# Kernel optimization log

Measured on AMD Instinct MI355X. Metric: run time of the kernel, lower is better.

The kernel has to match this reference:

```python
import jax, jax.numpy as jnp
import numpy as np

D = 1024

def _layernorm(x, gamma, beta, eps=1e-5):
    mu = jnp.mean(x, axis=-1, keepdims=True)
    var = jnp.var(x, axis=-1, keepdims=True)
    return (x - mu) * jax.lax.rsqrt(var + eps) * gamma + beta

def setup_inputs() -> dict:
    key = jax.random.key(0)
    ks = jax.random.split(key, 8)
    B, S = 4, 4096
    hidden_states = jax.random.normal(ks[0], (B, S, D), dtype=jnp.float32)
    attention_mask = jnp.ones((B, S), dtype=jnp.int32)  # unused by the module
    scale = 0.02
    Wq = jax.random.normal(ks[1], (D, D), jnp.float32) * scale
    bq = jnp.zeros((D,), jnp.float32)
    Wk = jax.random.normal(ks[2], (D, D), jnp.float32) * scale
    bk = jnp.zeros((D,), jnp.float32)
    Wv = jax.random.normal(ks[3], (D, D), jnp.float32) * scale
    bv = jnp.zeros((D,), jnp.float32)
    # query_att / key_att are initialized to weight=0, bias=1 in the module
    Wqa = jnp.zeros((D, D), jnp.float32)
    bqa = jnp.ones((D,), jnp.float32)
    Wka = jnp.zeros((D, D), jnp.float32)
    bka = jnp.ones((D,), jnp.float32)
    gamma = jnp.ones((D,), jnp.float32)
    beta = jnp.zeros((D,), jnp.float32)
    return {"hidden_states": hidden_states, "attention_mask": attention_mask,
            "Wq": Wq, "bq": bq, "Wqa": Wqa, "bqa": bqa,
            "Wk": Wk, "bk": bk, "Wka": Wka, "bka": bka,
            "Wv": Wv, "bv": bv, "gamma": gamma, "beta": beta}

def reference(hidden_states, attention_mask, Wq, bq, Wqa, bqa, Wk, bk, Wka, bka, Wv, bv, gamma, beta):
    h = _layernorm(hidden_states, gamma, beta)  # (B,S,D)
    B, S, d_model = h.shape
    inv_sqrt_d = 1.0 / jnp.sqrt(jnp.float32(d_model))
    query = h @ Wq + bq
    keys = h @ Wk + bk
    values = h @ Wv + bv
    # cumulative mean scaling: 1..S
    scaling = jnp.arange(1, S + 1, dtype=h.dtype).reshape(1, S, 1)
    query_weight = jax.nn.softmax((query @ Wqa + bqa) * inv_sqrt_d, axis=-1)
    pooled_query = jnp.cumsum(query_weight * query, axis=1) / scaling
    mixed_keys = pooled_query * keys
    keys_weight = jax.nn.softmax((mixed_keys @ Wka + bka) * inv_sqrt_d, axis=-1)
    pooled_keys = jnp.cumsum(keys_weight * mixed_keys, axis=1) / scaling
    return pooled_keys * values
```

## Files before the change

kernel.cpp:

```cpp
#include <hip/hip_runtime.h>

typedef _Float16 half_t;
typedef _Float16 f16x8 __attribute__((ext_vector_type(8)));
typedef _Float16 f16x4 __attribute__((ext_vector_type(4)));
typedef float f32x4 __attribute__((ext_vector_type(4)));

#define D_MODEL 1024
#define BS 4
#define SEQ 4096
#define ROWS (BS * SEQ)
#define SC 128
#define NC (SEQ / SC)

#define BARRIER() asm volatile("s_barrier" ::: "memory")
#define WAITV(n)  asm volatile("s_waitcnt vmcnt(" #n ")" ::: "memory")

__device__ __forceinline__ void gld_lds16(const half_t* g, char* l) {
  __builtin_amdgcn_global_load_lds((const __attribute__((address_space(1))) void*)g,
                                   (__attribute__((address_space(3))) void*)l, 16, 0, 0);
}

__global__ void zero_flags(int* f) {
  if (threadIdx.x < 2) f[threadIdx.x] = 0;
}

__global__ __launch_bounds__(256) void detect_nz(const float* __restrict__ W0,
                                                 const float* __restrict__ W1,
                                                 int* __restrict__ flags) {
  const int which = blockIdx.x >> 8;
  const unsigned* w = (const unsigned*)(which ? W1 : W0);
  const int blk = blockIdx.x & 255;
  unsigned v = 0;
  const size_t base = (size_t)blk * 4096 + threadIdx.x;
#pragma unroll
  for (int i = 0; i < 16; ++i) v |= w[base + i * 256];
#pragma unroll
  for (int off = 32; off > 0; off >>= 1) v |= __shfl_down(v, off, 64);
  __shared__ unsigned sv[4];
  if ((threadIdx.x & 63) == 0) sv[threadIdx.x >> 6] = v;
  __syncthreads();
  if (threadIdx.x == 0) {
    v = sv[0] | sv[1] | sv[2] | sv[3];
    if (v) atomicOr(&flags[which], 1);
  }
}

__global__ __launch_bounds__(256) void bias_softmax(const float* __restrict__ bqa,
                                                    const float* __restrict__ bka,
                                                    float* __restrict__ qwv,
                                                    float* __restrict__ kwv) {
  const float* b = blockIdx.x ? bka : bqa;
  float* o = blockIdx.x ? kwv : qwv;
  const int t = threadIdx.x;
  f32x4 v = *(const f32x4*)(b + t * 4);
  float x[4];
#pragma unroll
  for (int i = 0; i < 4; i++) x[i] = v[i] * 0.03125f;
  float mx = fmaxf(fmaxf(x[0], x[1]), fmaxf(x[2], x[3]));
#pragma unroll
  for (int off = 32; off > 0; off >>= 1) mx = fmaxf(mx, __shfl_xor(mx, off, 64));
  __shared__ float sm[4], ssum[4];
  const int wv = t >> 6, ln = t & 63;
  if (ln == 0) sm[wv] = mx;
  __syncthreads();
  mx = fmaxf(fmaxf(sm[0], sm[1]), fmaxf(sm[2], sm[3]));
  float e[4]; float s = 0.f;
#pragma unroll
  for (int i = 0; i < 4; i++) { e[i] = expf(x[i] - mx); s += e[i]; }
#pragma unroll
  for (int off = 32; off > 0; off >>= 1) s += __shfl_xor(s, off, 64);
  if (ln == 0) ssum[wv] = s;
  __syncthreads();
  s = ssum[0] + ssum[1] + ssum[2] + ssum[3];
  const float r = 1.0f / s;
  f32x4 ov;
#pragma unroll
  for (int i = 0; i < 4; i++) ov[i] = e[i] * r;
  *(f32x4*)(o + t * 4) = ov;
}

__global__ __launch_bounds__(256) void ln_kernel(const float* __restrict__ x,
                                                 const float* __restrict__ gamma,
                                                 const float* __restrict__ beta,
                                                 half_t* __restrict__ h) {
  const int row = blockIdx.x;
  const int t = threadIdx.x;
  const float* xr = x + (size_t)row * D_MODEL + t * 4;
  f32x4 v = *(const f32x4*)xr;
  float s = v[0] + v[1] + v[2] + v[3];
  float q = v[0]*v[0] + v[1]*v[1] + v[2]*v[2] + v[3]*v[3];
#pragma unroll
  for (int off = 32; off > 0; off >>= 1) {
    s += __shfl_down(s, off, 64);
    q += __shfl_down(q, off, 64);
  }
  __shared__ float rs[4], rq[4];
  const int wv = t >> 6, ln = t & 63;
  if (ln == 0) { rs[wv] = s; rq[wv] = q; }
  __syncthreads();
  s = rs[0] + rs[1] + rs[2] + rs[3];
  q = rq[0] + rq[1] + rq[2] + rq[3];
  const float mu = s * (1.0f / D_MODEL);
  const float var = q * (1.0f / D_MODEL) - mu * mu;
  const float rstd = rsqrtf(var + 1e-5f);
  f32x4 g = *(const f32x4*)(gamma + t * 4);
  f32x4 b = *(const f32x4*)(beta + t * 4);
  f16x4 o;
#pragma unroll
  for (int i = 0; i < 4; i++) o[i] = (half_t)((v[i] - mu) * rstd * g[i] + b[i]);
  *(f16x4*)(h + (size_t)row * D_MODEL + t * 4) = o;
}

__global__ __launch_bounds__(256) void prep_w(const float* __restrict__ Wq,
                                              const float* __restrict__ Wk,
                                              const float* __restrict__ Wv,
                                              const float* __restrict__ Wqa,
                                              const float* __restrict__ Wka,
                                              half_t* __restrict__ wcat,
                                              half_t* __restrict__ wqa,
                                              half_t* __restrict__ wka) {
  const int b = blockIdx.x;
  const int mat = b >> 10;
  const int tile = b & 1023;
  const int tn = (tile & 31) * 32;
  const int tk = (tile >> 5) * 32;
  const float* W = mat == 0 ? Wq : mat == 1 ? Wk : mat == 2 ? Wv : mat == 3 ? Wqa : Wka;
  half_t* dst = mat < 3 ? wcat + (size_t)mat * D_MODEL * D_MODEL : (mat == 3 ? wqa : wka);
  __shared__ float tl[32][33];
  const int tx = threadIdx.x & 31, ty = threadIdx.x >> 5;
#pragma unroll
  for (int i = 0; i < 32; i += 8)
    tl[ty + i][tx] = W[(size_t)(tk + ty + i) * D_MODEL + tn + tx];
  __syncthreads();
#pragma unroll
  for (int i = 0; i < 32; i += 8)
    dst[(size_t)(tn + ty + i) * D_MODEL + tk + tx] = (half_t)tl[tx][ty + i];
}

__global__ __launch_bounds__(256) void copy_bias(const float* __restrict__ bq,
                                                 const float* __restrict__ bk,
                                                 const float* __restrict__ bv,
                                                 float* __restrict__ bcat) {
  const int i = blockIdx.x * 256 + threadIdx.x;
  if (i < 1024) bcat[i] = bq[i];
  else if (i < 2048) bcat[i] = bk[i - 1024];
  else if (i < 3072) bcat[i] = bv[i - 2048];
}


#define STAGE_A(buf, h, kt) do { \
  gld_lds16(gA + (size_t)(h)*128*lda + (size_t)(kt)*64,        smem + (buf)*65536 + (h)*16384 + wid*1024); \
  gld_lds16(gA + ((size_t)(h)*128 + 64)*lda + (size_t)(kt)*64, smem + (buf)*65536 + (h)*16384 + 8192 + wid*1024); \
} while (0)

#define STAGE_B(buf, h, kt) do { \
  gld_lds16(gB + (size_t)(h)*128*1024 + (size_t)(kt)*64,        smem + (buf)*65536 + 32768 + (h)*16384 + wid*1024); \
  gld_lds16(gB + ((size_t)(h)*128 + 64)*1024 + (size_t)(kt)*64, smem + (buf)*65536 + 32768 + (h)*16384 + 8192 + wid*1024); \
} while (0)

#define LOAD_A(buf, base) do { \
  _Pragma("unroll") for (int _fm = 0; _fm < 4; ++_fm) { \
    aF[_fm][0] = *(const f16x8*)(smem + (buf)*65536 + rA + gsw0 + ((base)+_fm)*2048); \
    aF[_fm][1] = *(const f16x8*)(smem + (buf)*65536 + rA + gsw1 + ((base)+_fm)*2048); \
  } \
} while (0)

#define LOAD_B(dst, buf, base) do { \
  _Pragma("unroll") for (int _fn = 0; _fn < 2; ++_fn) { \
    dst[_fn][0] = *(const f16x8*)(smem + (buf)*65536 + 32768 + rB + gsw0 + ((base)+_fn)*2048); \
    dst[_fn][1] = *(const f16x8*)(smem + (buf)*65536 + 32768 + rB + gsw1 + ((base)+_fn)*2048); \
  } \
} while (0)

#define QUAD(BR, MOFF, NOFF) do { \
  __builtin_amdgcn_s_setprio(1); \
  _Pragma("unroll") for (int _fm = 0; _fm < 4; ++_fm) \
  _Pragma("unroll") for (int _fn = 0; _fn < 2; ++_fn) { \
    acc[(MOFF)+_fm][(NOFF)+_fn] = __builtin_amdgcn_mfma_f32_16x16x32_f16(aF[_fm][0], BR[_fn][0], acc[(MOFF)+_fm][(NOFF)+_fn], 0, 0, 0); \
    acc[(MOFF)+_fm][(NOFF)+_fn] = __builtin_amdgcn_mfma_f32_16x16x32_f16(aF[_fm][1], BR[_fn][1], acc[(MOFF)+_fm][(NOFF)+_fn], 0, 0, 0); \
  } \
  __builtin_amdgcn_s_setprio(0); \
} while (0)

__global__ __launch_bounds__(512, 2) void gemm8(const half_t* __restrict__ A, int lda,
                                                const half_t* __restrict__ Bt,
                                                const float* __restrict__ bias,
                                                half_t* __restrict__ C, int ldc,
                                                const int* skip) {
  if (skip && *skip == 0) return;
  extern __shared__ char smem[];
  const int t = threadIdx.x;
  const int ln = t & 63, wid = t >> 6;
  const int wm = wid >> 2, wn = wid & 3;

  const int gx = gridDim.x;
  const int nwg = gx * gridDim.y;
  const int orig = blockIdx.y * gx + blockIdx.x;
  const int swz = (orig & 7) * (nwg >> 3) + (orig >> 3);
  const int bx = swz % gx, by = swz / gx;
  const int n0 = bx * 256, m0 = by * 256;

  const int srow = t >> 3;
  const int sg = (t & 7) ^ (srow & 7);
  const half_t* gA = A + (size_t)(m0 + srow) * lda + sg * 8;
  const half_t* gB = Bt + (size_t)(n0 + srow) * 1024 + sg * 8;

  const int rA = (wm * 128 + (ln & 15)) * 128;
  const int rB = (wn * 64 + (ln & 15)) * 128;
  const int gsw0 = (((ln >> 4)) ^ (ln & 7)) << 4;
  const int gsw1 = ((4 | (ln >> 4)) ^ (ln & 7)) << 4;

  f32x4 acc[8][4] = {};
  f16x8 aF[4][2], bL[2][2], bH[2][2];

  STAGE_B(0, 0, 0); STAGE_B(0, 1, 0); STAGE_A(0, 0, 0); STAGE_A(0, 1, 0);
  STAGE_B(1, 0, 1); STAGE_B(1, 1, 1); STAGE_A(1, 0, 1); STAGE_A(1, 1, 1);
  WAITV(8); BARRIER();

#pragma unroll 1
  for (int i = 0; i < 8; ++i) {
    const int kc = 2 * i + 2;
    const int kd = 2 * i + 3;
    const bool f = (i < 7);
    LOAD_A(0, 0);
    LOAD_B(bL, 0, 0);
    BARRIER(); QUAD(bL, 0, 0); BARRIER();
    LOAD_B(bH, 0, 2);
    BARRIER(); QUAD(bH, 0, 2); BARRIER();
    LOAD_A(0, 4);
    if (f) { STAGE_B(0, 0, kc); STAGE_B(0, 1, kc); }
    BARRIER(); QUAD(bH, 4, 2); BARRIER();
    if (f) { STAGE_A(0, 0, kc); STAGE_A(0, 1, kc); WAITV(8); } else WAITV(0);
    BARRIER(); QUAD(bL, 4, 0); BARRIER();
    LOAD_A(1, 0);
    LOAD_B(bL, 1, 0);
    BARRIER(); QUAD(bL, 0, 0); BARRIER();
    LOAD_B(bH, 1, 2);
    BARRIER(); QUAD(bH, 0, 2); BARRIER();
    LOAD_A(1, 4);
    if (f) { STAGE_B(1, 0, kd); STAGE_B(1, 1, kd); }
    BARRIER(); QUAD(bH, 4, 2); BARRIER();
    if (f) { STAGE_A(1, 0, kd); STAGE_A(1, 1, kd); WAITV(8); } else WAITV(0);
    BARRIER(); QUAD(bL, 4, 0); BARRIER();
  }

  const int r0 = m0 + wm * 128 + ((ln >> 4) << 2);
  const int c0 = n0 + wn * 64 + (ln & 15);
  float bb[4];
#pragma unroll
  for (int fn = 0; fn < 4; ++fn) bb[fn] = bias[c0 + fn * 16];
#pragma unroll
  for (int fm = 0; fm < 8; ++fm)
#pragma unroll
    for (int fn = 0; fn < 4; ++fn) {
      const int col = c0 + fn * 16;
      const int row = r0 + fm * 16;
#pragma unroll
      for (int r = 0; r < 4; ++r)
        C[(size_t)(row + r) * ldc + col] = (half_t)(acc[fm][fn][r] + bb[fn]);
    }
}

__global__ __launch_bounds__(256) void softmax_k(const half_t* __restrict__ L,
                                                 half_t* __restrict__ O,
                                                 const int* skip) {
  if (skip && *skip == 0) return;
  const size_t row = blockIdx.x;
  const int t = threadIdx.x;
  f16x4 v = *(const f16x4*)(L + row * D_MODEL + t * 4);
  float x[4];
#pragma unroll
  for (int i = 0; i < 4; i++) x[i] = (float)v[i] * 0.03125f;
  float mx = fmaxf(fmaxf(x[0], x[1]), fmaxf(x[2], x[3]));
#pragma unroll
  for (int off = 32; off > 0; off >>= 1) mx = fmaxf(mx, __shfl_xor(mx, off, 64));
  __shared__ float sm[4], ssum[4];
  const int wv = t >> 6, ln = t & 63;
  if (ln == 0) sm[wv] = mx;
  __syncthreads();
  mx = fmaxf(fmaxf(sm[0], sm[1]), fmaxf(sm[2], sm[3]));
  float e[4]; float s = 0.f;
#pragma unroll
  for (int i = 0; i < 4; i++) { e[i] = expf(x[i] - mx); s += e[i]; }
#pragma unroll
  for (int off = 32; off > 0; off >>= 1) s += __shfl_xor(s, off, 64);
  if (ln == 0) ssum[wv] = s;
  __syncthreads();
  s = ssum[0] + ssum[1] + ssum[2] + ssum[3];
  const float r = 1.0f / s;
  f16x4 o;
#pragma unroll
  for (int i = 0; i < 4; i++) o[i] = (half_t)(e[i] * r);
  *(f16x4*)(O + row * D_MODEL + t * 4) = o;
}

__global__ __launch_bounds__(256) void cs_partial(const int* __restrict__ nz,
                                                  const float* __restrict__ wv,
                                                  const half_t* __restrict__ A, int ldA,
                                                  const half_t* __restrict__ B, int ldB,
                                                  float* __restrict__ part) {
  const int d = blockIdx.x * 256 + threadIdx.x;
  const int c = blockIdx.y;
  const int bb = blockIdx.z;
  const size_t s0 = (size_t)bb * SEQ + (size_t)c * SC;
  const half_t* pa = A + s0 * ldA + d;
  const half_t* pb = B + s0 * ldB + d;
  float acc = 0.f;
  if (*nz == 0) {
    const float w = wv[d];
#pragma unroll 8
    for (int s = 0; s < SC; s++) acc += w * (float)pb[(size_t)s * ldB];
  } else {
#pragma unroll 8
    for (int s = 0; s < SC; s++) acc += (float)pa[(size_t)s * ldA] * (float)pb[(size_t)s * ldB];
  }
  part[((size_t)bb * NC + c) * D_MODEL + d] = acc;
}

__global__ __launch_bounds__(256) void cs_partial2(const int* __restrict__ nz,
                                                   const float* __restrict__ wv,
                                                   const float* __restrict__ msum,
                                                   const half_t* __restrict__ A, int ldA,
                                                   const half_t* __restrict__ B, int ldB,
                                                   float* __restrict__ part) {
  const int d = blockIdx.x * 256 + threadIdx.x;
  const int c = blockIdx.y;
  const int bb = blockIdx.z;
  const size_t idx = ((size_t)bb * NC + c) * D_MODEL + d;
  if (*nz == 0) {
    part[idx] = wv[d] * msum[idx];
    return;
  }
  const size_t s0 = (size_t)bb * SEQ + (size_t)c * SC;
  const half_t* pa = A + s0 * ldA + d;
  const half_t* pb = B + s0 * ldB + d;
  float acc = 0.f;
#pragma unroll 8
  for (int s = 0; s < SC; s++) acc += (float)pa[(size_t)s * ldA] * (float)pb[(size_t)s * ldB];
  part[idx] = acc;
}

template <bool HALF_OUT>
__global__ __launch_bounds__(256) void cs_apply(const int* __restrict__ nz,
                                                const float* __restrict__ wv,
                                                const half_t* __restrict__ A, int ldA,
                                                const half_t* __restrict__ B, int ldB,
                                                const half_t* __restrict__ Cm, int ldC,
                                                const float* __restrict__ part,
                                                float* __restrict__ msum,
                                                half_t* __restrict__ OH,
                                                float* __restrict__ OF) {
  const int d = blockIdx.x * 256 + threadIdx.x;
  const int c = blockIdx.y;
  const int bb = blockIdx.z;
  float acc = 0.f;
  for (int cc = 0; cc < c; cc++) acc += part[((size_t)bb * NC + cc) * D_MODEL + d];
  const size_t s0 = (size_t)bb * SEQ + (size_t)c * SC;
  float ms = 0.f;
  if (*nz == 0) {
    const float w = wv[d];
#pragma unroll 4
    for (int s = 0; s < SC; s++) {
      const size_t sg = s0 + s;
      acc += w * (float)B[sg * ldB + d];
      const float pooled = acc / (float)(c * SC + s + 1);
      const float m = pooled * (float)Cm[sg * ldC + d];
      ms += m;
      if (HALF_OUT) OH[sg * D_MODEL + d] = (half_t)m;
      else          OF[sg * D_MODEL + d] = m;
    }
  } else {
#pragma unroll 4
    for (int s = 0; s < SC; s++) {
      const size_t sg = s0 + s;
      acc += (float)A[sg * ldA + d] * (float)B[sg * ldB + d];
      const float pooled = acc / (float)(c * SC + s + 1);
      const float m = pooled * (float)Cm[sg * ldC + d];
      ms += m;
      if (HALF_OUT) OH[sg * D_MODEL + d] = (half_t)m;
      else          OF[sg * D_MODEL + d] = m;
    }
  }
  if (msum) msum[((size_t)bb * NC + c) * D_MODEL + d] = ms;
}

extern "C" void kernel_launch(void* const* d_in, const int* in_sizes, int n_in,
                              void* d_out, int out_size, void* d_ws, size_t ws_size,
                              hipStream_t stream) {
  const float* x     = (const float*)d_in[0];
  const float* Wq    = (const float*)d_in[2];
  const float* bq    = (const float*)d_in[3];
  const float* Wqa   = (const float*)d_in[4];
  const float* bqa   = (const float*)d_in[5];
  const float* Wk    = (const float*)d_in[6];
  const float* bk    = (const float*)d_in[7];
  const float* Wka   = (const float*)d_in[8];
  const float* bka   = (const float*)d_in[9];
  const float* Wv    = (const float*)d_in[10];
  const float* bv    = (const float*)d_in[11];
  const float* gamma = (const float*)d_in[12];
  const float* beta  = (const float*)d_in[13];
  float* out = (float*)d_out;

  char* ws = (char*)d_ws;
  const size_t MB = 1024 * 1024;
  half_t* h16    = (half_t*)(ws + 0);
  half_t* qkv16  = (half_t*)(ws + 32 * MB);
  half_t* logits = (half_t*)(ws + 128 * MB);
  half_t* wcat   = (half_t*)(ws + 160 * MB);
  half_t* wqa16  = (half_t*)(ws + 166 * MB);
  half_t* wka16  = (half_t*)(ws + 168 * MB);
  float*  bcat   = (float*)(ws + 170 * MB);
  float*  part   = (float*)(ws + 170 * MB + 64 * 1024);
  float*  msum   = (float*)(ws + 170 * MB + 1024 * 1024);
  float*  qwv    = (float*)(ws + 170 * MB + 1600 * 1024);
  float*  kwv    = (float*)(ws + 170 * MB + 1604 * 1024);
  int*    flags  = (int*)(ws + 170 * MB + 1608 * 1024);

  half_t* q16 = qkv16;
  half_t* k16 = qkv16 + 1024;
  half_t* v16 = qkv16 + 2048;
  half_t* mixed16 = h16;
  half_t* sw = logits;

  hipFuncSetAttribute((const void*)gemm8, hipFuncAttributeMaxDynamicSharedMemorySize, 131072);

  zero_flags<<<1, 64, 0, stream>>>(flags);
  detect_nz<<<512, 256, 0, stream>>>(Wqa, Wka, flags);
  bias_softmax<<<2, 256, 0, stream>>>(bqa, bka, qwv, kwv);
  prep_w<<<5120, 256, 0, stream>>>(Wq, Wk, Wv, Wqa, Wka, wcat, wqa16, wka16);
  copy_bias<<<12, 256, 0, stream>>>(bq, bk, bv, bcat);
  ln_kernel<<<ROWS, 256, 0, stream>>>(x, gamma, beta, h16);
  gemm8<<<dim3(12, 64), 512, 131072, stream>>>(h16, 1024, wcat, bcat, qkv16, 3072, nullptr);
  gemm8<<<dim3(4, 64), 512, 131072, stream>>>(q16, 3072, wqa16, bqa, logits, 1024, flags);
  softmax_k<<<ROWS, 256, 0, stream>>>(logits, sw, flags);
  cs_partial<<<dim3(4, NC, BS), 256, 0, stream>>>(flags, qwv, sw, 1024, q16, 3072, part);
  cs_apply<true><<<dim3(4, NC, BS), 256, 0, stream>>>(flags, qwv, sw, 1024, q16, 3072,
                                                      k16, 3072, part, msum, mixed16, nullptr);
  gemm8<<<dim3(4, 64), 512, 131072, stream>>>(mixed16, 1024, wka16, bka, logits, 1024, flags + 1);
  softmax_k<<<ROWS, 256, 0, stream>>>(logits, sw, flags + 1);
  cs_partial2<<<dim3(4, NC, BS), 256, 0, stream>>>(flags + 1, kwv, msum, sw, 1024,
                                                   mixed16, 1024, part);
  cs_apply<false><<<dim3(4, NC, BS), 256, 0, stream>>>(flags + 1, kwv, sw, 1024, mixed16, 1024,
                                                       v16, 3072, part, nullptr, nullptr, out);
}
```

Baseline: 225.3 us.

## Interleave finer-grained global-to-LDS staging across GEMM compute phases

The GEMM's global-to-LDS prefetch is reorganised. Each wave now stages a contiguous 8-row group with a per-row XOR swizzle, and the A and B tile halves are issued in smaller pieces spread across all eight compute quads. Part of the next buffer's B tile is deferred into the following iteration, and the vmcnt waits are tightened to match. The aim is to overlap memory traffic more evenly with MFMA work and avoid bursts of outstanding loads. The cost is a more fragile dependency schedule between staging, waits and LDS reads.

```diff
diff --git a/kernel.cpp b/kernel.cpp
--- a/kernel.cpp
+++ b/kernel.cpp
@@ -148,14 +148,18 @@
 }
 
 
-#define STAGE_A(buf, h, kt) do { \
-  gld_lds16(gA + (size_t)(h)*128*lda + (size_t)(kt)*64,        smem + (buf)*65536 + (h)*16384 + wid*1024); \
-  gld_lds16(gA + ((size_t)(h)*128 + 64)*lda + (size_t)(kt)*64, smem + (buf)*65536 + (h)*16384 + 8192 + wid*1024); \
+#define SA2(buf, rb, kt) do { \
+  gld_lds16(gA + (size_t)((rb) + wbA + r8) * lda + (size_t)(kt) * 64 + grn * 8, \
+            smem + (buf)*65536 + ((rb) + wbA) * 128); \
+  gld_lds16(gA + (size_t)((rb) + 128 + wbA + r8) * lda + (size_t)(kt) * 64 + grn * 8, \
+            smem + (buf)*65536 + ((rb) + 128 + wbA) * 128); \
 } while (0)
 
-#define STAGE_B(buf, h, kt) do { \
-  gld_lds16(gB + (size_t)(h)*128*1024 + (size_t)(kt)*64,        smem + (buf)*65536 + 32768 + (h)*16384 + wid*1024); \
-  gld_lds16(gB + ((size_t)(h)*128 + 64)*1024 + (size_t)(kt)*64, smem + (buf)*65536 + 32768 + (h)*16384 + 8192 + wid*1024); \
+#define SB2(buf, gd, kt) do { \
+  gld_lds16(gB + (size_t)((gd) + wbB + r8) * 1024 + (size_t)(kt) * 64 + grn * 8, \
+            smem + (buf)*65536 + 32768 + ((gd) + wbB) * 128); \
+  gld_lds16(gB + (size_t)((gd) + 128 + wbB + r8) * 1024 + (size_t)(kt) * 64 + grn * 8, \
+            smem + (buf)*65536 + 32768 + ((gd) + 128 + wbB) * 128); \
 } while (0)
 
 #define LOAD_A(buf, base) do { \
@@ -200,10 +204,12 @@
   const int bx = swz % gx, by = swz / gx;
   const int n0 = bx * 256, m0 = by * 256;
 
-  const int srow = t >> 3;
-  const int sg = (t & 7) ^ (srow & 7);
-  const half_t* gA = A + (size_t)(m0 + srow) * lda + sg * 8;
-  const half_t* gB = Bt + (size_t)(n0 + srow) * 1024 + sg * 8;
+  const int r8 = (t >> 3) & 7;
+  const int grn = (t & 7) ^ r8;
+  const int wbA = wid * 8;
+  const int wbB = ((wid >> 2) << 6) + (wid & 3) * 8;
+  const half_t* gA = A + (size_t)m0 * lda;
+  const half_t* gB = Bt + (size_t)n0 * 1024;
 
   const int rA = (wm * 128 + (ln & 15)) * 128;
   const int rB = (wn * 64 + (ln & 15)) * 128;
@@ -213,34 +219,37 @@
   f32x4 acc[8][4] = {};
   f16x8 aF[4][2], bL[2][2], bH[2][2];
 
-  STAGE_B(0, 0, 0); STAGE_B(0, 1, 0); STAGE_A(0, 0, 0); STAGE_A(0, 1, 0);
-  STAGE_B(1, 0, 1); STAGE_B(1, 1, 1); STAGE_A(1, 0, 1); STAGE_A(1, 1, 1);
-  WAITV(8); BARRIER();
+  SA2(0, 0, 0); SB2(0, 0, 0); SA2(0, 64, 0); SB2(0, 32, 0);
+  SA2(1, 0, 1); SB2(1, 0, 1); SA2(1, 64, 1);
+  WAITV(6); BARRIER();
 
 #pragma unroll 1
   for (int i = 0; i < 8; ++i) {
+    const int kb = 2 * i + 1;
     const int kc = 2 * i + 2;
     const int kd = 2 * i + 3;
     const bool f = (i < 7);
-    LOAD_A(0, 0);
-    LOAD_B(bL, 0, 0);
+    LOAD_A(0, 0); LOAD_B(bL, 0, 0);
+    SB2(1, 32, kb);
     BARRIER(); QUAD(bL, 0, 0); BARRIER();
     LOAD_B(bH, 0, 2);
+    if (f) SA2(0, 0, kc);
     BARRIER(); QUAD(bH, 0, 2); BARRIER();
     LOAD_A(0, 4);
-    if (f) { STAGE_B(0, 0, kc); STAGE_B(0, 1, kc); }
+    if (f) SB2(0, 0, kc);
     BARRIER(); QUAD(bH, 4, 2); BARRIER();
-    if (f) { STAGE_A(0, 0, kc); STAGE_A(0, 1, kc); WAITV(8); } else WAITV(0);
+    if (f) { SA2(0, 64, kc); WAITV(6); } else WAITV(0);
     BARRIER(); QUAD(bL, 4, 0); BARRIER();
-    LOAD_A(1, 0);
-    LOAD_B(bL, 1, 0);
+    LOAD_A(1, 0); LOAD_B(bL, 1, 0);
+    if (f) SB2(0, 32, kc);
     BARRIER(); QUAD(bL, 0, 0); BARRIER();
     LOAD_B(bH, 1, 2);
+    if (f) SA2(1, 0, kd);
     BARRIER(); QUAD(bH, 0, 2); BARRIER();
     LOAD_A(1, 4);
-    if (f) { STAGE_B(1, 0, kd); STAGE_B(1, 1, kd); }
+    if (f) SB2(1, 0, kd);
     BARRIER(); QUAD(bH, 4, 2); BARRIER();
-    if (f) { STAGE_A(1, 0, kd); STAGE_A(1, 1, kd); WAITV(8); } else WAITV(0);
+    if (f) { SA2(1, 64, kd); WAITV(6); }
     BARRIER(); QUAD(bL, 4, 0); BARRIER();
   }
 
```

Measured after the change: 224.3 us. Within noise of the previous version (-0.4%).
